# Kernel tuning notes

Hardware: AMD Instinct MI355X
Metric: run time of the kernel (lower is better)

Reference implementation:

```python
import jax, jax.numpy as jnp
import numpy as np

EMBEDS = 512
HEADS = 4
HEAD_SIZE = 512  # head_size = embeds in Block.__init__
D_HEAD = EMBEDS // HEADS  # 128
LN_EPS = 512.0  # nn.LayerNorm(embeds, head_size) -> eps=head_size (faithful to source bug)
B, T = 4096, 4  # T must equal heads=4 for the mask broadcast in the source to work


def layer_norm(x, g, b, eps=LN_EPS):
    mu = jnp.mean(x, axis=-1, keepdims=True)
    var = jnp.mean(jnp.square(x - mu), axis=-1, keepdims=True)
    return (x - mu) / jnp.sqrt(var + eps) * g + b


def setup_inputs() -> dict:
    key = jax.random.key(0)
    ks = jax.random.split(key, 12)
    s_qkv = 1.0 / np.sqrt(D_HEAD)
    s_proj = 1.0 / np.sqrt(HEAD_SIZE)
    s_ff1 = 1.0 / np.sqrt(EMBEDS)
    s_ff2 = 1.0 / np.sqrt(4 * EMBEDS)
    return {
        "x": jax.random.normal(ks[0], (B, T, EMBEDS), dtype=jnp.float32),
        "Wq": jax.random.uniform(ks[1], (D_HEAD, HEAD_SIZE), jnp.float32, -s_qkv, s_qkv),
        "Wk": jax.random.uniform(ks[2], (D_HEAD, HEAD_SIZE), jnp.float32, -s_qkv, s_qkv),
        "Wv": jax.random.uniform(ks[3], (D_HEAD, HEAD_SIZE), jnp.float32, -s_qkv, s_qkv),
        "Wp": jax.random.uniform(ks[4], (HEAD_SIZE, EMBEDS), jnp.float32, -s_proj, s_proj),
        "bp": jax.random.uniform(ks[5], (EMBEDS,), jnp.float32, -s_proj, s_proj),
        "W1": jax.random.uniform(ks[6], (EMBEDS, 4 * EMBEDS), jnp.float32, -s_ff1, s_ff1),
        "b1": jax.random.uniform(ks[7], (4 * EMBEDS,), jnp.float32, -s_ff1, s_ff1),
        "W2": jax.random.uniform(ks[8], (4 * EMBEDS, EMBEDS), jnp.float32, -s_ff2, s_ff2),
        "b2": jax.random.uniform(ks[9], (EMBEDS,), jnp.float32, -s_ff2, s_ff2),
        "ln1_g": jnp.ones((EMBEDS,), jnp.float32),
        "ln1_b": jnp.zeros((EMBEDS,), jnp.float32),
        "ln2_g": jnp.ones((EMBEDS,), jnp.float32),
        "ln2_b": jnp.zeros((EMBEDS,), jnp.float32),
    }


def reference(x, Wq, Wk, Wv, Wp, bp, W1, b1, W2, b2, ln1_g, ln1_b, ln2_g, ln2_b):
    Bx, Tx, C = x.shape
    xh = x.reshape(Bx, Tx, HEADS, C // HEADS)          # [B,T,4,128]
    q = jnp.einsum('bthc,cd->bthd', xh, Wq)            # [B,T,4,512]
    k = jnp.einsum('bthc,cd->bthd', xh, Wk)
    v = jnp.einsum('bthc,cd->bthd', xh, Wv)
    # scores over the HEAD axis (faithful to source): [B,T,4,4]
    wei = jnp.einsum('btid,btjd->btij', q, k) * (HEAD_SIZE ** -0.5)
    causal = jnp.tril(jnp.ones((Tx, Tx), dtype=bool))  # broadcast over trailing [4,4]; requires T==4
    wei = jnp.where(causal, wei, -jnp.inf)
    wei = jax.nn.softmax(wei, axis=-1)                 # dropout omitted (eval mode)
    att = jnp.einsum('btij,btjd->btid', wei, v)        # [B,T,4,512]
    y = jnp.einsum('btid,de->btie', att, Wp) + bp      # [B,T,4,512]
    # residual broadcast: x [B,T,512] + y [B,T,4,512] -> [B,T,4,512]
    x1 = layer_norm(x[:, :, None, :] + y, ln1_g, ln1_b)
    h = jax.nn.gelu(jnp.einsum('btie,ef->btif', x1, W1) + b1, approximate=False)
    h = jnp.einsum('btif,fe->btie', h, W2) + b2
    return layer_norm(x1 + h, ln2_g, ln2_b)            # [B,T,4,512]
```

## Files before the change

### kernel.cpp

```cpp
#include <hip/hip_runtime.h>
#include <hip/hip_bf16.h>
#include <math.h>

typedef __bf16 bf16x8 __attribute__((ext_vector_type(8)));
typedef float f32x4 __attribute__((ext_vector_type(4)));
typedef unsigned short u16;
typedef unsigned int u32;
typedef u16 u16x4 __attribute__((ext_vector_type(4)));

#define TOKENS 16384
#define MROWS  65536

__device__ __forceinline__ u16 f2bf(float f) {
  union { __hip_bfloat16 h; u16 u; } c;
  c.h = __float2bfloat16(f);
  return c.u;
}
__device__ __forceinline__ float bf2f(u16 u) {
  union { u16 u; __hip_bfloat16 h; } c;
  c.u = u;
  return __bfloat162float(c.h);
}
__device__ __forceinline__ float gelu_f(float u) {
  float y2 = u * fmaf(0.07135481283f, u * u, 1.595769122f);
  float e = __expf(-y2);
  return u / (1.f + e);
}
__device__ __forceinline__ void gload16(const void* g, void* l) {
  __builtin_amdgcn_global_load_lds(
      (const __attribute__((address_space(1))) void*)g,
      (__attribute__((address_space(3))) void*)l, 16, 0, 0);
}

__global__ void kprep_G(const float* __restrict__ Wq, const float* __restrict__ Wk,
                        float* __restrict__ G) {
  int id = blockIdx.x * 256 + threadIdx.x;
  int c = id >> 7, c2 = id & 127;
  const float4* a = (const float4*)(Wq + (size_t)c * 512);
  const float4* b = (const float4*)(Wk + (size_t)c2 * 512);
  float s = 0.f;
#pragma unroll 8
  for (int i = 0; i < 128; ++i) {
    float4 xa = a[i], yb = b[i];
    s += xa.x * yb.x + xa.y * yb.y + xa.z * yb.z + xa.w * yb.w;
  }
  G[id] = s * 0.044194173824159216f;
}

__global__ void kprep_Wvp(const float* __restrict__ Wv, const float* __restrict__ Wp,
                          u16* __restrict__ WvpT) {
  int id = blockIdx.x * 256 + threadIdx.x;
  int e = id >> 7, c = id & 127;
  float s = 0.f;
#pragma unroll 4
  for (int d = 0; d < 512; ++d) s += Wv[(size_t)c * 512 + d] * Wp[(size_t)d * 512 + e];
  WvpT[id] = f2bf(s);
}

__global__ void kprep_W1T(const float* __restrict__ W1, u16* __restrict__ W1T) {
  int id = blockIdx.x * 256 + threadIdx.x;
  int f = id >> 9, e = id & 511;
  W1T[id] = f2bf(W1[(size_t)e * 2048 + f]);
}
__global__ void kprep_W2T(const float* __restrict__ W2, u16* __restrict__ W2T) {
  int id = blockIdx.x * 256 + threadIdx.x;
  int e = id >> 11, fst = id & 2047;
  int fb = fst >> 7, fs = fst & 127;
  int f_true = fb * 128 + ((fs >> 6) << 6) + ((fs & 3) << 4) + ((fs >> 2) & 15);
  W2T[id] = f2bf(W2[(size_t)f_true * 512 + e]);
}

__global__ __launch_bounds__(256) void ktoken(const float* __restrict__ x,
                                              const float* __restrict__ G,
                                              u16* __restrict__ Z) {
  __shared__ float Ss[4 * 512];
  __shared__ float T1s[4 * 512];
  __shared__ float Ws[4 * 16];
  int tid = threadIdx.x;
  int wave = tid >> 6, lane = tid & 63;
  int tok0 = blockIdx.x * 4;
  {
    const float4* xsrc = (const float4*)(x + (size_t)tok0 * 512);
    float4* sdst = (float4*)Ss;
    sdst[tid] = xsrc[tid];
    sdst[256 + tid] = xsrc[256 + tid];
  }
  __syncthreads();
  {
    const float* Sw = Ss + wave * 512;
    float a00 = 0, a01 = 0, a10 = 0, a11 = 0, a20 = 0, a21 = 0, a30 = 0, a31 = 0;
#pragma unroll 4
    for (int c = 0; c < 128; ++c) {
      float2 gg = ((const float2*)(G + (size_t)c * 128))[lane];
      float s0 = Sw[c], s1 = Sw[128 + c], s2 = Sw[256 + c], s3 = Sw[384 + c];
      a00 += s0 * gg.x; a01 += s0 * gg.y;
      a10 += s1 * gg.x; a11 += s1 * gg.y;
      a20 += s2 * gg.x; a21 += s2 * gg.y;
      a30 += s3 * gg.x; a31 += s3 * gg.y;
    }
    float* Tw = T1s + wave * 512;
    int c2 = lane * 2;
    Tw[c2] = a00; Tw[c2 + 1] = a01;
    Tw[128 + c2] = a10; Tw[128 + c2 + 1] = a11;
    Tw[256 + c2] = a20; Tw[256 + c2 + 1] = a21;
    Tw[384 + c2] = a30; Tw[384 + c2 + 1] = a31;
  }
  __syncthreads();
  if (lane < 16) {
    int i = lane >> 2, j = lane & 3;
    const float* Tw = T1s + wave * 512 + i * 128;
    const float* Sw = Ss + wave * 512 + j * 128;
    float d = 0.f;
#pragma unroll 8
    for (int c = 0; c < 128; ++c) d += Tw[c] * Sw[c];
    Ws[wave * 16 + i * 4 + j] = d;
  }
  __syncthreads();
  {
    float p[4][4];
    const float* ww = Ws + wave * 16;
#pragma unroll
    for (int i = 0; i < 4; ++i) {
      float m = -1e30f;
      for (int j = 0; j <= i; ++j) m = fmaxf(m, ww[i * 4 + j]);
      float s = 0.f;
      for (int j = 0; j <= i; ++j) { p[i][j] = __expf(ww[i * 4 + j] - m); s += p[i][j]; }
      float inv = 1.f / s;
      for (int j = 0; j <= i; ++j) p[i][j] *= inv;
      for (int j = i + 1; j < 4; ++j) p[i][j] = 0.f;
    }
    const float* Sw = Ss + wave * 512;
    int c = lane * 2;
    u32* zout = (u32*)(Z + (size_t)(tok0 + wave) * 512);
#pragma unroll
    for (int i = 0; i < 4; ++i) {
      float z0 = 0.f, z1 = 0.f;
#pragma unroll
      for (int j = 0; j < 4; ++j) {
        z0 += p[i][j] * Sw[j * 128 + c];
        z1 += p[i][j] * Sw[j * 128 + c + 1];
      }
      zout[i * 64 + lane] = (u32)f2bf(z0) | ((u32)f2bf(z1) << 16);
    }
  }
}

__global__ __launch_bounds__(512) void kattn(const u16* __restrict__ Z,
                                             const u16* __restrict__ WvpT,
                                             const float* __restrict__ bp,
                                             const float* __restrict__ x,
                                             const float* __restrict__ g1,
                                             const float* __restrict__ bln1,
                                             u16* __restrict__ X1) {
  __shared__ u16 AO[32768];
  __shared__ float rsum[64 * 4];
  __shared__ float rsq[64 * 4];
  __shared__ float mus[64];
  __shared__ float rss[64];
  char* smem = (char*)AO;
  int tid = threadIdx.x;
  int lane = tid & 63, wid = tid >> 6;
  int wm = wid >> 2, wnq = wid & 3;
  int lane_lo = lane & 15, lane_hi = lane >> 4;
  int m0 = blockIdx.x * 64;
  {
    const bf16x8* src = (const bf16x8*)(Z + (size_t)m0 * 128);
#pragma unroll
    for (int it = 0; it < 2; ++it) {
      int idx8 = it * 512 + tid;
      int row = idx8 >> 4;
      int byte = (idx8 * 16) ^ ((row & 7) << 4);
      *(bf16x8*)(smem + byte) = src[idx8];
    }
  }
  __syncthreads();
  f32x4 acc[2][8];
#pragma unroll
  for (int mi = 0; mi < 2; ++mi)
#pragma unroll
    for (int ni = 0; ni < 8; ++ni) acc[mi][ni] = (f32x4){0.f, 0.f, 0.f, 0.f};
#pragma unroll
  for (int ks = 0; ks < 4; ++ks) {
    bf16x8 af[2];
#pragma unroll
    for (int mi = 0; mi < 2; ++mi) {
      int row = wm * 32 + mi * 16 + lane_lo;
      int byte = (row * 256 + (ks * 32 + lane_hi * 8) * 2) ^ ((row & 7) << 4);
      af[mi] = *(const bf16x8*)(smem + byte);
    }
#pragma unroll
    for (int ni = 0; ni < 8; ++ni) {
      int n = wnq * 128 + ni * 16 + lane_lo;
      bf16x8 bfr = *(const bf16x8*)(WvpT + (size_t)n * 128 + ks * 32 + lane_hi * 8);
#pragma unroll
      for (int mi = 0; mi < 2; ++mi)
        acc[mi][ni] = __builtin_amdgcn_mfma_f32_16x16x32_bf16(af[mi], bfr, acc[mi][ni], 0, 0, 0);
    }
  }
#pragma unroll
  for (int mi = 0; mi < 2; ++mi) {
#pragma unroll
    for (int j = 0; j < 4; ++j) {
      int rl = wm * 32 + mi * 16 + lane_hi * 4 + j;
      int R = m0 + rl;
      const float* xrow = x + (size_t)(R >> 2) * 512;
      float s = 0.f, q = 0.f;
#pragma unroll
      for (int ni = 0; ni < 8; ++ni) {
        int col = wnq * 128 + ni * 16 + lane_lo;
        float val = acc[mi][ni][j] + bp[col] + xrow[col];
        acc[mi][ni][j] = val;
        s += val; q += val * val;
      }
#pragma unroll
      for (int off = 1; off < 16; off <<= 1) { s += __shfl_xor(s, off); q += __shfl_xor(q, off); }
      if (lane_lo == 0) { rsum[rl * 4 + wnq] = s; rsq[rl * 4 + wnq] = q; }
    }
  }
  __syncthreads();
  if (tid < 64) {
    float s = rsum[tid * 4] + rsum[tid * 4 + 1] + rsum[tid * 4 + 2] + rsum[tid * 4 + 3];
    float q = rsq[tid * 4] + rsq[tid * 4 + 1] + rsq[tid * 4 + 2] + rsq[tid * 4 + 3];
    float mu = s * (1.f / 512.f);
    float var = q * (1.f / 512.f) - mu * mu;
    mus[tid] = mu;
    rss[tid] = rsqrtf(var + 512.0f);
  }
  __syncthreads();
#pragma unroll
  for (int mi = 0; mi < 2; ++mi) {
#pragma unroll
    for (int j = 0; j < 4; ++j) {
      int rl = wm * 32 + mi * 16 + lane_hi * 4 + j;
      float mu = mus[rl], rs = rss[rl];
#pragma unroll
      for (int ni = 0; ni < 8; ++ni) {
        int col = wnq * 128 + ni * 16 + lane_lo;
        AO[rl * 512 + col] = f2bf((acc[mi][ni][j] - mu) * rs * g1[col] + bln1[col]);
      }
    }
  }
  __syncthreads();
  {
    bf16x8* dst = (bf16x8*)(X1 + (size_t)m0 * 512);
    const bf16x8* s8 = (const bf16x8*)AO;
#pragma unroll
    for (int it = 0; it < 8; ++it) dst[it * 512 + tid] = s8[it * 512 + tid];
  }
}

template<int KDIM>
__device__ __forceinline__ void gemm_core_sb(const u16* __restrict__ Ap,
                                             const u16* __restrict__ Bp,
                                             u16* Ab, u16* Bb,
                                             int wid, int lane, f32x4 acc[4][4]) {
  const int lane_lo = lane & 15, lane_hi = lane >> 4;
  const int wm = wid >> 1, wn = wid & 1;
  const int rl8 = lane >> 3, u8 = lane & 7;
  char* AbC = (char*)Ab;
  char* BbC = (char*)Bb;
  for (int k0 = 0; k0 < KDIM; k0 += 64) {
#pragma unroll
    for (int i = 0; i < 4; ++i) {
      int row = wid * 32 + i * 8 + rl8;
      int usw = u8 ^ (row & 7);
      size_t goff = (size_t)row * KDIM + k0 + usw * 8;
      gload16(Ap + goff, AbC + wid * 4096 + i * 1024);
      gload16(Bp + goff, BbC + wid * 4096 + i * 1024);
    }
    __syncthreads();
#pragma unroll
    for (int ks = 0; ks < 2; ++ks) {
      bf16x8 av[4], bv[4];
#pragma unroll
      for (int mi = 0; mi < 4; ++mi) {
        int row = wm * 64 + mi * 16 + lane_lo;
        int usw = (ks * 4 + lane_hi) ^ (row & 7);
        av[mi] = *(const bf16x8*)(AbC + row * 128 + usw * 16);
      }
#pragma unroll
      for (int ni = 0; ni < 4; ++ni) {
        int row = wn * 64 + ni * 16 + lane_lo;
        int usw = (ks * 4 + lane_hi) ^ (row & 7);
        bv[ni] = *(const bf16x8*)(BbC + row * 128 + usw * 16);
      }
#pragma unroll
      for (int mi = 0; mi < 4; ++mi)
#pragma unroll
        for (int ni = 0; ni < 4; ++ni)
          acc[mi][ni] = __builtin_amdgcn_mfma_f32_16x16x32_bf16(av[mi], bv[ni], acc[mi][ni], 0, 0, 0);
    }
    __syncthreads();
  }
}

template<int KDIM>
__device__ __forceinline__ void gemm_core_db(const u16* __restrict__ Ap,
                                             const u16* __restrict__ Bp,
                                             u16* AbBase, u16* BbBase,
                                             int wid, int lane, f32x4 acc[4][4]) {
  const int lane_lo = lane & 15, lane_hi = lane >> 4;
  const int wm = wid >> 1, wn = wid & 1;
  const int rl8 = lane >> 3, u8 = lane & 7;

  auto stage = [&](int buf, int k0) {
    char* AbC = (char*)AbBase + buf * 16384;
    char* BbC = (char*)BbBase + buf * 16384;
#pragma unroll
    for (int i = 0; i < 4; ++i) {
      int row = wid * 32 + i * 8 + rl8;
      int usw = u8 ^ (row & 7);
      size_t goff = (size_t)row * KDIM + k0 + usw * 8;
      gload16(Ap + goff, AbC + wid * 4096 + i * 1024);
      gload16(Bp + goff, BbC + wid * 4096 + i * 1024);
    }
  };
  auto compute = [&](int buf) {
    char* AbC = (char*)AbBase + buf * 16384;
    char* BbC = (char*)BbBase + buf * 16384;
#pragma unroll
    for (int ks = 0; ks < 2; ++ks) {
      bf16x8 av[4], bv[4];
#pragma unroll
      for (int mi = 0; mi < 4; ++mi) {
        int row = wm * 64 + mi * 16 + lane_lo;
        int usw = (ks * 4 + lane_hi) ^ (row & 7);
        av[mi] = *(const bf16x8*)(AbC + row * 128 + usw * 16);
      }
#pragma unroll
      for (int ni = 0; ni < 4; ++ni) {
        int row = wn * 64 + ni * 16 + lane_lo;
        int usw = (ks * 4 + lane_hi) ^ (row & 7);
        bv[ni] = *(const bf16x8*)(BbC + row * 128 + usw * 16);
      }
#pragma unroll
      for (int mi = 0; mi < 4; ++mi)
#pragma unroll
        for (int ni = 0; ni < 4; ++ni)
          acc[mi][ni] = __builtin_amdgcn_mfma_f32_16x16x32_bf16(av[mi], bv[ni], acc[mi][ni], 0, 0, 0);
    }
  };

  stage(0, 0);
  asm volatile("s_waitcnt vmcnt(0)" ::: "memory");
  __builtin_amdgcn_s_barrier();
  __builtin_amdgcn_sched_barrier(0);
  int cur = 0;
  for (int k0 = 64; k0 < KDIM; k0 += 64) {
    stage(cur ^ 1, k0);
    compute(cur);
    asm volatile("s_waitcnt vmcnt(0)" ::: "memory");
    __builtin_amdgcn_s_barrier();
    __builtin_amdgcn_sched_barrier(0);
    cur ^= 1;
  }
  compute(cur);
}

__global__ __launch_bounds__(256) void kff1(const u16* __restrict__ X1s,
                                            const u16* __restrict__ W1T,
                                            const float* __restrict__ b1v,
                                            u16* __restrict__ H) {
  __shared__ __align__(16) u16 Ab[8192];
  __shared__ __align__(16) u16 Bb[8192];
  int tid = threadIdx.x, lane = tid & 63, wid = tid >> 6;
  int nwg = gridDim.x, bid = blockIdx.x;
  int m128 = nwg >> 4;
  int xcd = bid & 7, idx = bid >> 3;
  int mb = xcd * (m128 >> 3) + (idx >> 4);
  int nb = idx & 15;
  const u16* Ap = X1s + (size_t)mb * 128 * 512;
  const u16* Bp = W1T + (size_t)nb * 128 * 512;
  f32x4 acc[4][4];
#pragma unroll
  for (int mi = 0; mi < 4; ++mi)
#pragma unroll
    for (int ni = 0; ni < 4; ++ni) acc[mi][ni] = (f32x4){0.f, 0.f, 0.f, 0.f};
  gemm_core_sb<512>(Ap, Bp, Ab, Bb, wid, lane, acc);
  int lane_lo = lane & 15, lane_hi = lane >> 4;
  int wm = wid >> 1, wn = wid & 1;
  float bvals[4];
#pragma unroll
  for (int ni = 0; ni < 4; ++ni) bvals[ni] = b1v[nb * 128 + wn * 64 + ni * 16 + lane_lo];
  int colb = nb * 128 + (wn * 16 + lane_lo) * 4;
#pragma unroll
  for (int mi = 0; mi < 4; ++mi)
#pragma unroll
    for (int j = 0; j < 4; ++j) {
      int rl = wm * 64 + mi * 16 + lane_hi * 4 + j;
      u16x4 pk;
#pragma unroll
      for (int ni = 0; ni < 4; ++ni)
        pk[ni] = f2bf(gelu_f(acc[mi][ni][j] + bvals[ni]));
      *(u16x4*)(H + ((size_t)mb * 128 + rl) * 2048 + colb) = pk;
    }
}

__global__ __launch_bounds__(256) void kff2(const u16* __restrict__ H,
                                            const u16* __restrict__ W2T,
                                            const float* __restrict__ b2v,
                                            const u16* __restrict__ X1s,
                                            float* __restrict__ Ps) {
  __shared__ __align__(16) u16 Ab[16384];
  __shared__ __align__(16) u16 Bb[16384];
  int tid = threadIdx.x, lane = tid & 63, wid = tid >> 6;
  int nwg = gridDim.x, bid = blockIdx.x;
  int m128 = nwg >> 2;
  int xcd = bid & 7, idx = bid >> 3;
  int mb = xcd * (m128 >> 3) + (idx >> 2);
  int nb = idx & 3;
  const u16* Ap = H + (size_t)mb * 128 * 2048;
  const u16* Bp = W2T + (size_t)nb * 128 * 2048;
  f32x4 acc[4][4];
#pragma unroll
  for (int mi = 0; mi < 4; ++mi)
#pragma unroll
    for (int ni = 0; ni < 4; ++ni) acc[mi][ni] = (f32x4){0.f, 0.f, 0.f, 0.f};
  gemm_core_db<2048>(Ap, Bp, Ab, Bb, wid, lane, acc);
  int lane_lo = lane & 15, lane_hi = lane >> 4;
  int wm = wid >> 1, wn = wid & 1;
#pragma unroll
  for (int mi = 0; mi < 4; ++mi)
#pragma unroll
    for (int j = 0; j < 4; ++j) {
      int rl = wm * 64 + mi * 16 + lane_hi * 4 + j;
      size_t row = (size_t)mb * 128 + rl;
      const u16* xrow = X1s + row * 512 + nb * 128;
      float* prow = Ps + row * 512 + nb * 128;
#pragma unroll
      for (int ni = 0; ni < 4; ++ni) {
        int col = wn * 64 + ni * 16 + lane_lo;
        prow[col] = acc[mi][ni][j] + b2v[nb * 128 + col] + bf2f(xrow[col]);
      }
    }
}

__global__ __launch_bounds__(512) void kln2(float* __restrict__ P,
                                            const float* __restrict__ g2,
                                            const float* __restrict__ bb2) {
  int wid = threadIdx.x >> 6, lane = threadIdx.x & 63;
  size_t row = (size_t)blockIdx.x * 8 + wid;
  float* pr = P + row * 512;
  float4 v0 = *(float4*)(pr + lane * 4);
  float4 v1 = *(float4*)(pr + 256 + lane * 4);
  float s = v0.x + v0.y + v0.z + v0.w + v1.x + v1.y + v1.z + v1.w;
  float q = v0.x * v0.x + v0.y * v0.y + v0.z * v0.z + v0.w * v0.w +
            v1.x * v1.x + v1.y * v1.y + v1.z * v1.z + v1.w * v1.w;
#pragma unroll
  for (int off = 1; off < 64; off <<= 1) { s += __shfl_xor(s, off); q += __shfl_xor(q, off); }
  float mu = s * (1.f / 512.f);
  float rs = rsqrtf(q * (1.f / 512.f) - mu * mu + 512.0f);
  float4 ga = *(const float4*)(g2 + lane * 4);
  float4 gb = *(const float4*)(g2 + 256 + lane * 4);
  float4 ba = *(const float4*)(bb2 + lane * 4);
  float4 bb = *(const float4*)(bb2 + 256 + lane * 4);
  v0.x = (v0.x - mu) * rs * ga.x + ba.x;
  v0.y = (v0.y - mu) * rs * ga.y + ba.y;
  v0.z = (v0.z - mu) * rs * ga.z + ba.z;
  v0.w = (v0.w - mu) * rs * ga.w + ba.w;
  v1.x = (v1.x - mu) * rs * gb.x + bb.x;
  v1.y = (v1.y - mu) * rs * gb.y + bb.y;
  v1.z = (v1.z - mu) * rs * gb.z + bb.z;
  v1.w = (v1.w - mu) * rs * gb.w + bb.w;
  *(float4*)(pr + lane * 4) = v0;
  *(float4*)(pr + 256 + lane * 4) = v1;
}

extern "C" void kernel_launch(void* const* d_in, const int* in_sizes, int n_in,
                              void* d_out, int out_size, void* d_ws, size_t ws_size,
                              hipStream_t stream) {
  const float* x   = (const float*)d_in[0];
  const float* Wq  = (const float*)d_in[1];
  const float* Wk  = (const float*)d_in[2];
  const float* Wv  = (const float*)d_in[3];
  const float* Wp  = (const float*)d_in[4];
  const float* bp  = (const float*)d_in[5];
  const float* W1  = (const float*)d_in[6];
  const float* b1  = (const float*)d_in[7];
  const float* W2  = (const float*)d_in[8];
  const float* b2  = (const float*)d_in[9];
  const float* g1  = (const float*)d_in[10];
  const float* bb1 = (const float*)d_in[11];
  const float* g2  = (const float*)d_in[12];
  const float* bb2 = (const float*)d_in[13];
  float* out = (float*)d_out;

  char* ws = (char*)d_ws;
  float* G  = (float*)ws;
  u16* WvpT = (u16*)(ws + (256 << 10));
  u16* W1T  = (u16*)(ws + (1 << 20));
  u16* W2T  = (u16*)(ws + (3 << 20));
  u16* Z    = (u16*)(ws + (5 << 20));
  u16* X1   = (u16*)(ws + (21 << 20));
  u16* H    = (u16*)(ws + (85ull << 20));

  hipLaunchKernelGGL(kprep_G,   dim3(64),   dim3(256), 0, stream, Wq, Wk, G);
  hipLaunchKernelGGL(kprep_Wvp, dim3(256),  dim3(256), 0, stream, Wv, Wp, WvpT);
  hipLaunchKernelGGL(kprep_W1T, dim3(4096), dim3(256), 0, stream, W1, W1T);
  hipLaunchKernelGGL(kprep_W2T, dim3(4096), dim3(256), 0, stream, W2, W2T);
  hipLaunchKernelGGL(ktoken,    dim3(4096), dim3(256), 0, stream, x, G, Z);
  hipLaunchKernelGGL(kattn,     dim3(1024), dim3(512), 0, stream, Z, WvpT, bp, x, g1, bb1, X1);

  const size_t hbase = 85ull << 20;
  int S = 64;
  for (int c = 4; c <= 64; c <<= 1) {
    if (hbase + (268435456ull / (size_t)c) <= ws_size) { S = c; break; }
  }
  int Ms = MROWS / S;
  for (int s = 0; s < S; ++s) {
    const u16* x1s = X1 + (size_t)s * Ms * 512;
    float* outs = out + (size_t)s * Ms * 512;
    hipLaunchKernelGGL(kff1, dim3((Ms / 128) * 16), dim3(256), 0, stream, x1s, W1T, b1, H);
    hipLaunchKernelGGL(kff2, dim3((Ms / 128) * 4),  dim3(256), 0, stream, H, W2T, b2, x1s, outs);
  }
  hipLaunchKernelGGL(kln2, dim3(8192), dim3(512), 0, stream, out, g2, bb2);
}
```

Baseline: 676.4 us.

## Tile weight transposes through LDS and stage bf16 G in LDS for token kernel

Weight transpose kernels for W1 and W2 now use 64x64 LDS tiles, so global reads are coalesced float4 loads and writes are 16-byte vectors instead of strided scalar accesses. The Gram matrix G is stored in bf16 and loaded into LDS once per block with global_load_lds. The token kernel now computes the 4x4 head scores with wave-level shuffle reductions instead of extra LDS round trips and block barriers. Storing G in bf16 lowers the precision of the attention scores and adds a 32KB LDS footprint per block, which may reduce occupancy.

```diff
diff --git a/kernel.cpp b/kernel.cpp
--- a/kernel.cpp
+++ b/kernel.cpp
@@ -7,6 +7,7 @@
 typedef unsigned short u16;
 typedef unsigned int u32;
 typedef u16 u16x4 __attribute__((ext_vector_type(4)));
+typedef u16 u16x8 __attribute__((ext_vector_type(8)));
 
 #define TOKENS 16384
 #define MROWS  65536
@@ -33,7 +34,7 @@
 }
 
 __global__ void kprep_G(const float* __restrict__ Wq, const float* __restrict__ Wk,
-                        float* __restrict__ G) {
+                        u16* __restrict__ Gbf) {
   int id = blockIdx.x * 256 + threadIdx.x;
   int c = id >> 7, c2 = id & 127;
   const float4* a = (const float4*)(Wq + (size_t)c * 512);
@@ -44,7 +45,7 @@
     float4 xa = a[i], yb = b[i];
     s += xa.x * yb.x + xa.y * yb.y + xa.z * yb.z + xa.w * yb.w;
   }
-  G[id] = s * 0.044194173824159216f;
+  Gbf[id] = f2bf(s * 0.044194173824159216f);
 }
 
 __global__ void kprep_Wvp(const float* __restrict__ Wv, const float* __restrict__ Wp,
@@ -57,91 +58,126 @@
   WvpT[id] = f2bf(s);
 }
 
-__global__ void kprep_W1T(const float* __restrict__ W1, u16* __restrict__ W1T) {
-  int id = blockIdx.x * 256 + threadIdx.x;
-  int f = id >> 9, e = id & 511;
-  W1T[id] = f2bf(W1[(size_t)e * 2048 + f]);
-}
-__global__ void kprep_W2T(const float* __restrict__ W2, u16* __restrict__ W2T) {
-  int id = blockIdx.x * 256 + threadIdx.x;
-  int e = id >> 11, fst = id & 2047;
-  int fb = fst >> 7, fs = fst & 127;
-  int f_true = fb * 128 + ((fs >> 6) << 6) + ((fs & 3) << 4) + ((fs >> 2) & 15);
-  W2T[id] = f2bf(W2[(size_t)f_true * 512 + e]);
+__global__ __launch_bounds__(256) void kprep_W1T(const float* __restrict__ W1,
+                                                 u16* __restrict__ W1T) {
+  __shared__ u16 Lt[64][72];
+  int tid = threadIdx.x;
+  int bf = blockIdx.x, be = blockIdx.y;
+#pragma unroll
+  for (int rnd = 0; rnd < 4; ++rnd) {
+    int r = rnd * 16 + (tid >> 4);
+    int f4 = (tid & 15) * 4;
+    float4 v = *(const float4*)(W1 + (size_t)(be * 64 + r) * 2048 + bf * 64 + f4);
+    Lt[r][f4] = f2bf(v.x); Lt[r][f4 + 1] = f2bf(v.y);
+    Lt[r][f4 + 2] = f2bf(v.z); Lt[r][f4 + 3] = f2bf(v.w);
+  }
+  __syncthreads();
+  int fl = tid >> 2, eg = (tid & 3) * 16;
+  u16x8 o0, o1;
+#pragma unroll
+  for (int q = 0; q < 8; ++q) { o0[q] = Lt[eg + q][fl]; o1[q] = Lt[eg + 8 + q][fl]; }
+  u16* dst = W1T + (size_t)(bf * 64 + fl) * 512 + be * 64 + eg;
+  *(u16x8*)dst = o0;
+  *(u16x8*)(dst + 8) = o1;
+}
+
+__global__ __launch_bounds__(256) void kprep_W2T(const float* __restrict__ W2,
+                                                 u16* __restrict__ W2T) {
+  __shared__ u16 Lt[64][72];
+  int tid = threadIdx.x;
+  int bf = blockIdx.x, be = blockIdx.y;
+#pragma unroll
+  for (int rnd = 0; rnd < 4; ++rnd) {
+    int r = rnd * 16 + (tid >> 4);
+    int e4 = (tid & 15) * 4;
+    float4 v = *(const float4*)(W2 + (size_t)(bf * 64 + r) * 512 + be * 64 + e4);
+    Lt[r][e4] = f2bf(v.x); Lt[r][e4 + 1] = f2bf(v.y);
+    Lt[r][e4 + 2] = f2bf(v.z); Lt[r][e4 + 3] = f2bf(v.w);
+  }
+  __syncthreads();
+  int aa = bf & 1, fb = bf >> 1;
+  int el = tid >> 2, g = tid & 3;
+  u16x8 o0, o1;
+#pragma unroll
+  for (int q = 0; q < 8; ++q) {
+    int fs0 = g * 16 + q, fs1 = g * 16 + 8 + q;
+    o0[q] = Lt[(fs0 & 3) * 16 + ((fs0 >> 2) & 15)][el];
+    o1[q] = Lt[(fs1 & 3) * 16 + ((fs1 >> 2) & 15)][el];
+  }
+  u16* dst = W2T + (size_t)(be * 64 + el) * 2048 + fb * 128 + aa * 64 + g * 16;
+  *(u16x8*)dst = o0;
+  *(u16x8*)(dst + 8) = o1;
 }
 
 __global__ __launch_bounds__(256) void ktoken(const float* __restrict__ x,
-                                              const float* __restrict__ G,
+                                              const u16* __restrict__ Gbf,
                                               u16* __restrict__ Z) {
   __shared__ float Ss[4 * 512];
-  __shared__ float T1s[4 * 512];
-  __shared__ float Ws[4 * 16];
+  __shared__ __align__(16) u16 Gs[16384];
   int tid = threadIdx.x;
   int wave = tid >> 6, lane = tid & 63;
-  int tok0 = blockIdx.x * 4;
+  int tok = blockIdx.x * 4 + wave;
+  char* GsC = (char*)Gs;
+#pragma unroll
+  for (int it = 0; it < 8; ++it)
+    gload16(Gbf + (size_t)(it * 256 + tid) * 8, GsC + it * 4096 + wave * 1024);
   {
-    const float4* xsrc = (const float4*)(x + (size_t)tok0 * 512);
-    float4* sdst = (float4*)Ss;
-    sdst[tid] = xsrc[tid];
-    sdst[256 + tid] = xsrc[256 + tid];
-  }
-  __syncthreads();
-  {
-    const float* Sw = Ss + wave * 512;
-    float a00 = 0, a01 = 0, a10 = 0, a11 = 0, a20 = 0, a21 = 0, a30 = 0, a31 = 0;
+    const float4* xs = (const float4*)(x + (size_t)tok * 512);
+    float4* sw = (float4*)(Ss + wave * 512);
+    sw[lane] = xs[lane];
+    sw[64 + lane] = xs[64 + lane];
+  }
+  __syncthreads();
+
+  const float* Sw = Ss + wave * 512;
+  const u32* Grow = (const u32*)Gs;
+  float a[4][2] = {{0.f, 0.f}, {0.f, 0.f}, {0.f, 0.f}, {0.f, 0.f}};
 #pragma unroll 4
-    for (int c = 0; c < 128; ++c) {
-      float2 gg = ((const float2*)(G + (size_t)c * 128))[lane];
-      float s0 = Sw[c], s1 = Sw[128 + c], s2 = Sw[256 + c], s3 = Sw[384 + c];
-      a00 += s0 * gg.x; a01 += s0 * gg.y;
-      a10 += s1 * gg.x; a11 += s1 * gg.y;
-      a20 += s2 * gg.x; a21 += s2 * gg.y;
-      a30 += s3 * gg.x; a31 += s3 * gg.y;
-    }
-    float* Tw = T1s + wave * 512;
-    int c2 = lane * 2;
-    Tw[c2] = a00; Tw[c2 + 1] = a01;
-    Tw[128 + c2] = a10; Tw[128 + c2 + 1] = a11;
-    Tw[256 + c2] = a20; Tw[256 + c2 + 1] = a21;
-    Tw[384 + c2] = a30; Tw[384 + c2 + 1] = a31;
-  }
-  __syncthreads();
-  if (lane < 16) {
-    int i = lane >> 2, j = lane & 3;
-    const float* Tw = T1s + wave * 512 + i * 128;
-    const float* Sw = Ss + wave * 512 + j * 128;
-    float d = 0.f;
-#pragma unroll 8
-    for (int c = 0; c < 128; ++c) d += Tw[c] * Sw[c];
-    Ws[wave * 16 + i * 4 + j] = d;
-  }
-  __syncthreads();
-  {
-    float p[4][4];
-    const float* ww = Ws + wave * 16;
-#pragma unroll
-    for (int i = 0; i < 4; ++i) {
-      float m = -1e30f;
-      for (int j = 0; j <= i; ++j) m = fmaxf(m, ww[i * 4 + j]);
-      float s = 0.f;
-      for (int j = 0; j <= i; ++j) { p[i][j] = __expf(ww[i * 4 + j] - m); s += p[i][j]; }
-      float inv = 1.f / s;
-      for (int j = 0; j <= i; ++j) p[i][j] *= inv;
-      for (int j = i + 1; j < 4; ++j) p[i][j] = 0.f;
-    }
-    const float* Sw = Ss + wave * 512;
-    int c = lane * 2;
-    u32* zout = (u32*)(Z + (size_t)(tok0 + wave) * 512);
-#pragma unroll
-    for (int i = 0; i < 4; ++i) {
-      float z0 = 0.f, z1 = 0.f;
-#pragma unroll
-      for (int j = 0; j < 4; ++j) {
-        z0 += p[i][j] * Sw[j * 128 + c];
-        z1 += p[i][j] * Sw[j * 128 + c + 1];
-      }
-      zout[i * 64 + lane] = (u32)f2bf(z0) | ((u32)f2bf(z1) << 16);
-    }
+  for (int c = 0; c < 128; ++c) {
+    u32 g2 = Grow[c * 64 + lane];
+    float glo = __uint_as_float(g2 << 16);
+    float ghi = __uint_as_float(g2 & 0xFFFF0000u);
+    float s0 = Sw[c], s1 = Sw[128 + c], s2 = Sw[256 + c], s3 = Sw[384 + c];
+    a[0][0] += s0 * glo; a[0][1] += s0 * ghi;
+    a[1][0] += s1 * glo; a[1][1] += s1 * ghi;
+    a[2][0] += s2 * glo; a[2][1] += s2 * ghi;
+    a[3][0] += s3 * glo; a[3][1] += s3 * ghi;
+  }
+  float w[16];
+#pragma unroll
+  for (int j = 0; j < 4; ++j) {
+    float sj0 = Sw[j * 128 + 2 * lane];
+    float sj1 = Sw[j * 128 + 2 * lane + 1];
+#pragma unroll
+    for (int i = 0; i < 4; ++i)
+      w[i * 4 + j] = a[i][0] * sj0 + a[i][1] * sj1;
+  }
+#pragma unroll
+  for (int off = 1; off < 64; off <<= 1)
+#pragma unroll
+    for (int k = 0; k < 16; ++k) w[k] += __shfl_xor(w[k], off);
+  float p[4][4];
+#pragma unroll
+  for (int i = 0; i < 4; ++i) {
+    float m = w[i * 4];
+    for (int j = 1; j <= i; ++j) m = fmaxf(m, w[i * 4 + j]);
+    float s = 0.f;
+    for (int j = 0; j <= i; ++j) { p[i][j] = __expf(w[i * 4 + j] - m); s += p[i][j]; }
+    float inv = 1.f / s;
+    for (int j = 0; j <= i; ++j) p[i][j] *= inv;
+    for (int j = i + 1; j < 4; ++j) p[i][j] = 0.f;
+  }
+  int c = lane * 2;
+  u32* zout = (u32*)(Z + (size_t)tok * 512);
+#pragma unroll
+  for (int i = 0; i < 4; ++i) {
+    float z0 = 0.f, z1 = 0.f;
+#pragma unroll
+    for (int j = 0; j < 4; ++j) {
+      z0 += p[i][j] * Sw[j * 128 + c];
+      z1 += p[i][j] * Sw[j * 128 + c + 1];
+    }
+    zout[i * 64 + lane] = (u32)f2bf(z0) | ((u32)f2bf(z1) << 16);
   }
 }
 
@@ -486,7 +522,7 @@
   float* out = (float*)d_out;
 
   char* ws = (char*)d_ws;
-  float* G  = (float*)ws;
+  u16* Gbf  = (u16*)ws;
   u16* WvpT = (u16*)(ws + (256 << 10));
   u16* W1T  = (u16*)(ws + (1 << 20));
   u16* W2T  = (u16*)(ws + (3 << 20));
@@ -494,12 +530,12 @@
   u16* X1   = (u16*)(ws + (21 << 20));
   u16* H    = (u16*)(ws + (85ull << 20));
 
-  hipLaunchKernelGGL(kprep_G,   dim3(64),   dim3(256), 0, stream, Wq, Wk, G);
-  hipLaunchKernelGGL(kprep_Wvp, dim3(256),  dim3(256), 0, stream, Wv, Wp, WvpT);
-  hipLaunchKernelGGL(kprep_W1T, dim3(4096), dim3(256), 0, stream, W1, W1T);
-  hipLaunchKernelGGL(kprep_W2T, dim3(4096), dim3(256), 0, stream, W2, W2T);
-  hipLaunchKernelGGL(ktoken,    dim3(4096), dim3(256), 0, stream, x, G, Z);
-  hipLaunchKernelGGL(kattn,     dim3(1024), dim3(512), 0, stream, Z, WvpT, bp, x, g1, bb1, X1);
+  hipLaunchKernelGGL(kprep_G,   dim3(64),        dim3(256), 0, stream, Wq, Wk, Gbf);
+  hipLaunchKernelGGL(kprep_Wvp, dim3(256),       dim3(256), 0, stream, Wv, Wp, WvpT);
+  hipLaunchKernelGGL(kprep_W1T, dim3(32, 8),     dim3(256), 0, stream, W1, W1T);
+  hipLaunchKernelGGL(kprep_W2T, dim3(32, 8),     dim3(256), 0, stream, W2, W2T);
+  hipLaunchKernelGGL(ktoken,    dim3(4096),      dim3(256), 0, stream, x, Gbf, Z);
+  hipLaunchKernelGGL(kattn,     dim3(1024),      dim3(512), 0, stream, Z, WvpT, bp, x, g1, bb1, X1);
 
   const size_t hbase = 85ull << 20;
   int S = 64;
```

Result: faster. 631.8 us (-6.6%).
